# Performance work log

Measured on AMD Instinct MI355X. Metric: run time of the kernel, lower is better.

Reference implementation:

```python
import jax, jax.numpy as jnp
import numpy as np

N = 100000   # nodes
E = 3200000  # edges (avg degree 32)
F_IN = 128   # node feature dim (lazy in_channels)
C = 16       # GAT out_channels, heads=1
ED = 2       # edge_dim
B = 512      # graphs in batch
OUT_X = 64; OUT_Y = 64; ROT = 4
EPS = 1e-5


def _bn(x, g, b):
    # BatchNorm1d in training mode: biased batch variance, eps=1e-5
    mu = x.mean(0, keepdims=True)
    var = x.var(0, keepdims=True)
    return g * (x - mu) * jax.lax.rsqrt(var + EPS) + b


def _gat(x, src, dst, edge_attr, W, We, att_s, att_d, att_e, bias):
    # PyG GATConv, heads=1: self-loops added with fill_value='mean' edge attrs
    n = x.shape[0]
    deg = jax.ops.segment_sum(jnp.ones_like(dst, jnp.float32), dst, num_segments=n)
    loop_attr = jax.ops.segment_sum(edge_attr, dst, num_segments=n) / jnp.maximum(deg, 1.0)[:, None]
    idx = jnp.arange(n)
    src_f = jnp.concatenate([src, idx])
    dst_f = jnp.concatenate([dst, idx])
    ea = jnp.concatenate([edge_attr, loop_attr], axis=0)  # [E+N, ED]
    h = x @ W                      # [N, C]
    a_s = h @ att_s                # [N]
    a_d = h @ att_d                # [N]
    a_e = (ea @ We) @ att_e        # [E+N]
    logits = jax.nn.leaky_relu(a_s[src_f] + a_d[dst_f] + a_e, 0.2)
    m = jax.ops.segment_max(logits, dst_f, num_segments=n)  # every node has a self-loop
    ex = jnp.exp(logits - m[dst_f])
    alpha = ex / jax.ops.segment_sum(ex, dst_f, num_segments=n)[dst_f]
    return jax.ops.segment_sum(alpha[:, None] * h[src_f], dst_f, num_segments=n) + bias


def _glorot(k, shp):
    lim = float(np.sqrt(6.0 / (shp[0] + shp[1])))
    return jax.random.uniform(k, shp, jnp.float32, -lim, lim)


def setup_inputs() -> dict:
    key = jax.random.key(0)
    k = jax.random.split(key, 48)
    d = {}
    d['x'] = jax.random.normal(k[0], (N, F_IN), jnp.float32)
    d['edge_index'] = jax.random.randint(k[1], (2, E), 0, N)
    d['edge_attr'] = jax.random.normal(k[2], (E, ED), jnp.float32)
    d['batch'] = jnp.sort(jax.random.randint(k[3], (N,), 0, B))
    # gat1
    d['W1'] = _glorot(k[4], (F_IN, C)); d['We1'] = _glorot(k[5], (ED, C))
    d['as1'] = 0.1 * jax.random.normal(k[6], (C,)); d['ad1'] = 0.1 * jax.random.normal(k[7], (C,))
    d['ae1'] = 0.1 * jax.random.normal(k[8], (C,)); d['b1'] = jnp.zeros((C,), jnp.float32)
    # norm1 (BatchNorm on nodes)
    d['g1'] = 1.0 + 0.1 * jax.random.normal(k[9], (C,)); d['bb1'] = 0.1 * jax.random.normal(k[10], (C,))
    # gat2
    d['W2'] = _glorot(k[11], (C, C)); d['We2'] = _glorot(k[12], (ED, C))
    d['as2'] = 0.1 * jax.random.normal(k[13], (C,)); d['ad2'] = 0.1 * jax.random.normal(k[14], (C,))
    d['ae2'] = 0.1 * jax.random.normal(k[15], (C,)); d['b2'] = jnp.zeros((C,), jnp.float32)
    # D2RL MLP tail
    d['gL1'] = 1.0 + 0.1 * jax.random.normal(k[16], (C,)); d['bL1'] = 0.1 * jax.random.normal(k[17], (C,))
    d['Wl1'] = _glorot(k[18], (C, C)); d['bl1'] = 0.1 * jax.random.normal(k[19], (C,))
    d['gL2'] = 1.0 + 0.1 * jax.random.normal(k[20], (2 * C,)); d['bL2'] = 0.1 * jax.random.normal(k[21], (2 * C,))
    d['Wl2'] = _glorot(k[22], (2 * C, C)); d['bl2'] = 0.1 * jax.random.normal(k[23], (C,))
    d['gL3'] = 1.0 + 0.1 * jax.random.normal(k[24], (2 * C,)); d['bL3'] = 0.1 * jax.random.normal(k[25], (2 * C,))
    d['Wl3'] = _glorot(k[26], (2 * C, C)); d['bl3'] = 0.1 * jax.random.normal(k[27], (C,))
    d['Wx'] = _glorot(k[28], (C, OUT_X)); d['bx'] = 0.1 * jax.random.normal(k[29], (OUT_X,))
    d['Wy'] = _glorot(k[30], (C, OUT_Y)); d['by'] = 0.1 * jax.random.normal(k[31], (OUT_Y,))
    d['Wr'] = _glorot(k[32], (C, ROT)); d['br'] = 0.1 * jax.random.normal(k[33], (ROT,))
    return d


def reference(x, edge_index, edge_attr, batch,
              W1, We1, as1, ad1, ae1, b1, g1, bb1,
              W2, We2, as2, ad2, ae2, b2,
              gL1, bL1, Wl1, bl1, gL2, bL2, Wl2, bl2, gL3, bL3, Wl3, bl3,
              Wx, bx, Wy, by, Wr, br):
    src, dst = edge_index[0], edge_index[1]
    h = jax.nn.relu(_gat(x, src, dst, edge_attr, W1, We1, as1, ad1, ae1, b1))
    h = _bn(h, g1, bb1)
    h = jax.nn.relu(_gat(h, src, dst, edge_attr, W2, We2, as2, ad2, ae2, b2))
    # MeanAggregation over graphs
    cnt = jax.ops.segment_sum(jnp.ones((h.shape[0],), jnp.float32), batch, num_segments=B)
    xe = jax.ops.segment_sum(h, batch, num_segments=B) / jnp.maximum(cnt, 1.0)[:, None]  # [B, C]
    z = _bn(xe, gL1, bL1)
    z = jax.nn.relu(z @ Wl1 + bl1)
    z = _bn(jnp.concatenate([z, xe], axis=1), gL2, bL2)
    z = jax.nn.relu(z @ Wl2 + bl2)
    z = _bn(jnp.concatenate([z, xe], axis=1), gL3, bL3)
    z = jax.nn.relu(z @ Wl3 + bl3)
    xx = jax.nn.softmax(z @ Wx + bx, axis=1)
    y = jax.nn.softmax(z @ Wy + by, axis=1)
    rot = jax.nn.softmax(z @ Wr + br, axis=1)
    return (xx, y, rot)
```

## Files before the change

### kernel.cpp

```cpp
#include <hip/hip_runtime.h>
#include <hip/hip_fp16.h>
#include <math.h>

#define C 16
#define FIN 128

typedef unsigned int u32x2 __attribute__((ext_vector_type(2)));

__global__ __launch_bounds__(256) void k_gemm1(
    const float* __restrict__ x, const float* __restrict__ W,
    const float* __restrict__ asw, const float* __restrict__ adw,
    __half* __restrict__ hh, float* __restrict__ a_s, float* __restrict__ a_d, int n) {
  __shared__ float xs[64 * 129];
  __shared__ float Ws[FIN * C];
  __shared__ float pAs[4][64], pAd[4][64];
  int t = threadIdx.x;
  int node0 = blockIdx.x * 64;
  for (int i = t; i < FIN * C; i += 256) Ws[i] = W[i];
  for (int i = t; i < 64 * FIN; i += 256) {
    int r = i >> 7, c = i & 127;
    int node = node0 + r;
    xs[r * 129 + c] = (node < n) ? x[(size_t)node * FIN + c] : 0.f;
  }
  __syncthreads();
  int nn = t & 63, cg = (t >> 6) * 4, grp = t >> 6;
  float a0 = 0.f, a1 = 0.f, a2 = 0.f, a3 = 0.f;
  const float* xr = &xs[nn * 129];
  #pragma unroll 8
  for (int k = 0; k < FIN; ++k) {
    float xv = xr[k];
    const float* wr = &Ws[k * C + cg];
    a0 += xv * wr[0]; a1 += xv * wr[1]; a2 += xv * wr[2]; a3 += xv * wr[3];
  }
  int node = node0 + nn;
  if (node < n) {
    __half2 p0 = __floats2half2_rn(a0, a1), p1 = __floats2half2_rn(a2, a3);
    unsigned u0, u1;
    memcpy(&u0, &p0, 4); memcpy(&u1, &p1, 4);
    *(uint2*)(hh + (size_t)node * 16 + cg) = make_uint2(u0, u1);
  }
  pAs[grp][nn] = a0 * asw[cg] + a1 * asw[cg + 1] + a2 * asw[cg + 2] + a3 * asw[cg + 3];
  pAd[grp][nn] = a0 * adw[cg] + a1 * adw[cg + 1] + a2 * adw[cg + 2] + a3 * adw[cg + 3];
  __syncthreads();
  if (t < 64 && node0 + t < n) {
    a_s[node0 + t] = pAs[0][t] + pAs[1][t] + pAs[2][t] + pAs[3][t];
    a_d[node0 + t] = pAd[0][t] + pAd[1][t] + pAd[2][t] + pAd[3][t];
  }
}

__global__ __launch_bounds__(256) void k_hist_rank(
    const int* __restrict__ dst, int* __restrict__ counts,
    int* __restrict__ rank, int ne) {
  int e = blockIdx.x * 256 + threadIdx.x;
  if (e < ne) rank[e] = atomicAdd(&counts[dst[e]], 1);
}

__global__ __launch_bounds__(512) void k_scan1(const int* __restrict__ counts,
                                               int* __restrict__ bsum, int n) {
  __shared__ int sd[512];
  int i = blockIdx.x * 512 + threadIdx.x;
  sd[threadIdx.x] = (i < n) ? counts[i] : 0;
  __syncthreads();
  for (int s = 256; s > 0; s >>= 1) {
    if (threadIdx.x < s) sd[threadIdx.x] += sd[threadIdx.x + s];
    __syncthreads();
  }
  if (threadIdx.x == 0) bsum[blockIdx.x] = sd[0];
}

__global__ __launch_bounds__(512) void k_scan2(int* __restrict__ bsum,
                                               int* __restrict__ offs,
                                               int nblk, int n) {
  __shared__ int sd[512];
  int t = threadIdx.x;
  int v = (t < nblk) ? bsum[t] : 0;
  sd[t] = v;
  __syncthreads();
  for (int off = 1; off < 512; off <<= 1) {
    int x = (t >= off) ? sd[t - off] : 0;
    __syncthreads();
    sd[t] += x;
    __syncthreads();
  }
  if (t < nblk) bsum[t] = sd[t] - v;
  if (t == nblk - 1) offs[n] = sd[t];
}

__global__ __launch_bounds__(512) void k_scan3(const int* __restrict__ counts,
                                               const int* __restrict__ bsum,
                                               int* __restrict__ offs, int n) {
  __shared__ int sd[512];
  int t = threadIdx.x;
  int i = blockIdx.x * 512 + t;
  int v = (i < n) ? counts[i] : 0;
  sd[t] = v;
  __syncthreads();
  for (int off = 1; off < 512; off <<= 1) {
    int x = (t >= off) ? sd[t - off] : 0;
    __syncthreads();
    sd[t] += x;
    __syncthreads();
  }
  if (i < n) offs[i] = bsum[blockIdx.x] + sd[t] - v;
}

__global__ __launch_bounds__(256) void k_scatter(
    const int* __restrict__ src, const int* __restrict__ dst,
    const float2* __restrict__ ea, const int* __restrict__ offs,
    const int* __restrict__ rank,
    const float* __restrict__ We1, const float* __restrict__ ae1,
    const float* __restrict__ We2, const float* __restrict__ ae2,
    uint2* __restrict__ bucket, int ne) {
  int e = blockIdx.x * 256 + threadIdx.x;
  if (e >= ne) return;
  float w01 = 0.f, w11 = 0.f, w02 = 0.f, w12 = 0.f;
  #pragma unroll
  for (int c = 0; c < C; ++c) {
    w01 += We1[c] * ae1[c]; w11 += We1[C + c] * ae1[c];
    w02 += We2[c] * ae2[c]; w12 += We2[C + c] * ae2[c];
  }
  int d = dst[e];
  float2 a = ea[e];
  __half2 hp = __floats2half2_rn(a.x * w01 + a.y * w11, a.x * w02 + a.y * w12);
  unsigned hb;
  memcpy(&hb, &hp, 4);
  bucket[offs[d] + rank[e]] = make_uint2((unsigned)src[e], hb);
}

__global__ __launch_bounds__(256) void k_gather(
    const uint2* __restrict__ bucket, const int* __restrict__ offs,
    const float* __restrict__ a_s, const float* __restrict__ a_d,
    const __half* __restrict__ hh, const float* __restrict__ bias,
    float* __restrict__ outv, float* __restrict__ bnsum, float* __restrict__ bnsq,
    int lay, int do_bn, int n) {
  __shared__ float sbn[32];
  int t = threadIdx.x;
  if (t < 32) sbn[t] = 0.f;
  __syncthreads();

  int node = blockIdx.x * 16 + (t >> 4);
  int l = t & 15, f = l & 1, p = l >> 1;

  float acc[8];
  #pragma unroll
  for (int j = 0; j < 8; ++j) acc[j] = 0.f;
  float den = 0.f, ssum = 0.f;
  int o0 = 0, o1 = 0;
  float adi = 0.f, asi = 0.f;
  if (node < n) {
    o0 = offs[node]; o1 = offs[node + 1];
    adi = a_d[node]; asi = a_s[node];
    int e = o0 + p;
    u32x2 r = {0u, 0u};
    if (e < o1) r = __builtin_nontemporal_load((const u32x2*)(bucket + e));
    while (e < o1) {
      int en = e + 8;
      u32x2 rn = {0u, 0u};
      if (en < o1) rn = __builtin_nontemporal_load((const u32x2*)(bucket + en));
      int s = (int)r.x;
      unsigned scb = r.y;
      __half2 sc2;
      memcpy(&sc2, &scb, 4);
      float se = lay ? __high2float(sc2) : __low2float(sc2);
      float asv = a_s[s];
      uint4 hv = *(const uint4*)(hh + ((size_t)s << 4) + (f << 3));
      float lg = asv + adi + se;
      lg = lg > 0.f ? lg : 0.2f * lg;
      float ex = __expf(lg);
      den += ex; ssum += se;
      __half2 t0, t1, t2, t3;
      memcpy(&t0, &hv.x, 4); memcpy(&t1, &hv.y, 4);
      memcpy(&t2, &hv.z, 4); memcpy(&t3, &hv.w, 4);
      float2 g0 = __half22float2(t0), g1 = __half22float2(t1);
      float2 g2 = __half22float2(t2), g3 = __half22float2(t3);
      acc[0] += ex * g0.x; acc[1] += ex * g0.y;
      acc[2] += ex * g1.x; acc[3] += ex * g1.y;
      acc[4] += ex * g2.x; acc[5] += ex * g2.y;
      acc[6] += ex * g3.x; acc[7] += ex * g3.y;
      r = rn; e = en;
    }
  }
  #pragma unroll
  for (int off = 2; off <= 8; off <<= 1) {
    den += __shfl_xor(den, off);
    ssum += __shfl_xor(ssum, off);
    #pragma unroll
    for (int j = 0; j < 8; ++j) acc[j] += __shfl_xor(acc[j], off);
  }

  float v[8];
  #pragma unroll
  for (int j = 0; j < 8; ++j) v[j] = 0.f;
  if (node < n) {
    float dgc = fmaxf((float)(o1 - o0), 1.f);
    float lg = asi + adi + ssum / dgc;
    lg = lg > 0.f ? lg : 0.2f * lg;
    float exs = __expf(lg);
    uint4 hv = *(const uint4*)(hh + ((size_t)node << 4) + (f << 3));
    __half2 t0, t1, t2, t3;
    memcpy(&t0, &hv.x, 4); memcpy(&t1, &hv.y, 4);
    memcpy(&t2, &hv.z, 4); memcpy(&t3, &hv.w, 4);
    float2 g0 = __half22float2(t0), g1 = __half22float2(t1);
    float2 g2 = __half22float2(t2), g3 = __half22float2(t3);
    float hs[8] = {g0.x, g0.y, g1.x, g1.y, g2.x, g2.y, g3.x, g3.y};
    float inv = 1.f / (den + exs);
    const float* bp = bias + f * 8;
    #pragma unroll
    for (int j = 0; j < 8; ++j)
      v[j] = fmaxf((acc[j] + exs * hs[j]) * inv + bp[j], 0.f);
    if (p == 0) {
      float4* op = (float4*)(outv + ((size_t)node << 4));
      op[f * 2]     = make_float4(v[0], v[1], v[2], v[3]);
      op[f * 2 + 1] = make_float4(v[4], v[5], v[6], v[7]);
    }
  }

  if (do_bn) {
    float sv[8], qv[8];
    bool act = (node < n) && (p == 0);
    #pragma unroll
    for (int j = 0; j < 8; ++j) {
      sv[j] = act ? v[j] : 0.f;
      qv[j] = sv[j] * sv[j];
    }
    #pragma unroll
    for (int j = 0; j < 8; ++j) {
      sv[j] += __shfl_down(sv[j], 32); qv[j] += __shfl_down(qv[j], 32);
      sv[j] += __shfl_down(sv[j], 16); qv[j] += __shfl_down(qv[j], 16);
    }
    if ((t & 63) < 2) {
      #pragma unroll
      for (int j = 0; j < 8; ++j) {
        atomicAdd(&sbn[f * 8 + j], sv[j]);
        atomicAdd(&sbn[16 + f * 8 + j], qv[j]);
      }
    }
    __syncthreads();
    if (t < 16) atomicAdd(&bnsum[t], sbn[t]);
    else if (t < 32) atomicAdd(&bnsq[t - 16], sbn[t]);
  }
}

__global__ void k_bnp(const float* __restrict__ bnsum, const float* __restrict__ bnsq,
                      const float* __restrict__ g, const float* __restrict__ bb,
                      float* __restrict__ scale, float* __restrict__ shift, float invn) {
  int c = threadIdx.x;
  if (c >= C) return;
  float mean = bnsum[c] * invn;
  float var = bnsq[c] * invn - mean * mean;
  float s = g[c] * rsqrtf(var + 1e-5f);
  scale[c] = s; shift[c] = bb[c] - mean * s;
}

__global__ __launch_bounds__(256) void k_node2(
    const float* __restrict__ outv, const float* __restrict__ scale,
    const float* __restrict__ shift, const float* __restrict__ W2,
    const float* __restrict__ asw, const float* __restrict__ adw,
    __half* __restrict__ hh, float* __restrict__ a_s, float* __restrict__ a_d, int n) {
  __shared__ float w2s[C * C];
  if (threadIdx.x < C * C) w2s[threadIdx.x] = W2[threadIdx.x];
  __syncthreads();
  int i = blockIdx.x * 256 + threadIdx.x;
  if (i >= n) return;
  float hn[C];
  #pragma unroll
  for (int c = 0; c < C; ++c) hn[c] = outv[(size_t)i * C + c] * scale[c] + shift[c];
  float h2[C];
  #pragma unroll
  for (int j = 0; j < C; ++j) {
    float acc = 0.f;
    #pragma unroll
    for (int c = 0; c < C; ++c) acc += hn[c] * w2s[c * C + j];
    h2[j] = acc;
  }
  float hs = 0.f, hd = 0.f;
  #pragma unroll
  for (int j = 0; j < C; ++j) { hs += h2[j] * asw[j]; hd += h2[j] * adw[j]; }
  a_s[i] = hs; a_d[i] = hd;
  unsigned wbits[8];
  #pragma unroll
  for (int j = 0; j < 8; ++j) {
    __half2 hq = __floats2half2_rn(h2[2 * j], h2[2 * j + 1]);
    memcpy(&wbits[j], &hq, 4);
  }
  uint4* hp = (uint4*)(hh + (size_t)i * 16);
  hp[0] = make_uint4(wbits[0], wbits[1], wbits[2], wbits[3]);
  hp[1] = make_uint4(wbits[4], wbits[5], wbits[6], wbits[7]);
}

__global__ void k_gstart(const int* __restrict__ batch, int* __restrict__ gs,
                         int n, int B_) {
  int g = blockIdx.x * blockDim.x + threadIdx.x;
  if (g > B_) return;
  if (g == B_) { gs[B_] = n; return; }
  int lo = 0, hi = n;
  while (lo < hi) { int mid = (lo + hi) >> 1; if (batch[mid] < g) lo = mid + 1; else hi = mid; }
  gs[g] = lo;
}

__global__ __launch_bounds__(256) void k_xe(
    const float* __restrict__ outv, const int* __restrict__ gs,
    float* __restrict__ xe, int B_) {
  int wave = blockIdx.x * 4 + (threadIdx.x >> 6);
  if (wave >= B_) return;
  int lane = threadIdx.x & 63;
  int c = lane & 15, sub = lane >> 4;
  int base = gs[wave], end = gs[wave + 1];
  float s = 0.f;
  for (int n0 = base + sub; n0 < end; n0 += 4) s += outv[(size_t)n0 * C + c];
  s += __shfl_down(s, 32);
  s += __shfl_down(s, 16);
  if (lane < 16) xe[(size_t)wave * C + c] = s / fmaxf((float)(end - base), 1.f);
}

__global__ __launch_bounds__(512) void k_tail_z3(
    const float* __restrict__ xe_in,
    const float* __restrict__ gL1, const float* __restrict__ bL1,
    const float* __restrict__ Wl1, const float* __restrict__ bl1,
    const float* __restrict__ gL2, const float* __restrict__ bL2,
    const float* __restrict__ Wl2, const float* __restrict__ bl2,
    const float* __restrict__ gL3, const float* __restrict__ bL3,
    const float* __restrict__ Wl3, const float* __restrict__ bl3,
    float* __restrict__ z3buf, int B_) {
  __shared__ float ssum[2 * C], ssq[2 * C], sc[2 * C], sh[2 * C];
  int t = threadIdx.x;
  float invB = 1.f / (float)B_;
  float xe[C];
  #pragma unroll
  for (int c = 0; c < C; ++c) xe[c] = xe_in[(size_t)t * C + c];

  if (t < 2 * C) { ssum[t] = 0.f; ssq[t] = 0.f; }
  __syncthreads();
  #pragma unroll
  for (int c = 0; c < C; ++c) {
    float s = xe[c], q = xe[c] * xe[c];
    for (int o = 32; o > 0; o >>= 1) { s += __shfl_down(s, o); q += __shfl_down(q, o); }
    if ((t & 63) == 0) { atomicAdd(&ssum[c], s); atomicAdd(&ssq[c], q); }
  }
  __syncthreads();
  if (t < C) {
    float mean = ssum[t] * invB, var = ssq[t] * invB - mean * mean;
    float s = gL1[t] * rsqrtf(var + 1e-5f);
    sc[t] = s; sh[t] = bL1[t] - mean * s;
  }
  __syncthreads();
  float z[C];
  #pragma unroll
  for (int j = 0; j < C; ++j) {
    float acc = bl1[j];
    #pragma unroll
    for (int c = 0; c < C; ++c) acc += (xe[c] * sc[c] + sh[c]) * Wl1[c * C + j];
    z[j] = fmaxf(acc, 0.f);
  }
  __syncthreads();

  if (t < 2 * C) { ssum[t] = 0.f; ssq[t] = 0.f; }
  __syncthreads();
  #pragma unroll
  for (int c = 0; c < C; ++c) {
    float s = z[c], q = z[c] * z[c];
    for (int o = 32; o > 0; o >>= 1) { s += __shfl_down(s, o); q += __shfl_down(q, o); }
    if ((t & 63) == 0) { atomicAdd(&ssum[c], s); atomicAdd(&ssq[c], q); }
    float s2 = xe[c], q2 = xe[c] * xe[c];
    for (int o = 32; o > 0; o >>= 1) { s2 += __shfl_down(s2, o); q2 += __shfl_down(q2, o); }
    if ((t & 63) == 0) { atomicAdd(&ssum[C + c], s2); atomicAdd(&ssq[C + c], q2); }
  }
  __syncthreads();
  if (t < 2 * C) {
    float mean = ssum[t] * invB, var = ssq[t] * invB - mean * mean;
    float s = gL2[t] * rsqrtf(var + 1e-5f);
    sc[t] = s; sh[t] = bL2[t] - mean * s;
  }
  __syncthreads();
  float z2[C];
  #pragma unroll
  for (int j = 0; j < C; ++j) {
    float acc = bl2[j];
    #pragma unroll
    for (int c = 0; c < C; ++c) acc += (z[c] * sc[c] + sh[c]) * Wl2[c * C + j];
    #pragma unroll
    for (int c = 0; c < C; ++c) acc += (xe[c] * sc[C + c] + sh[C + c]) * Wl2[(C + c) * C + j];
    z2[j] = fmaxf(acc, 0.f);
  }
  __syncthreads();

  if (t < 2 * C) { ssum[t] = 0.f; ssq[t] = 0.f; }
  __syncthreads();
  #pragma unroll
  for (int c = 0; c < C; ++c) {
    float s = z2[c], q = z2[c] * z2[c];
    for (int o = 32; o > 0; o >>= 1) { s += __shfl_down(s, o); q += __shfl_down(q, o); }
    if ((t & 63) == 0) { atomicAdd(&ssum[c], s); atomicAdd(&ssq[c], q); }
    float s2 = xe[c], q2 = xe[c] * xe[c];
    for (int o = 32; o > 0; o >>= 1) { s2 += __shfl_down(s2, o); q2 += __shfl_down(q2, o); }
    if ((t & 63) == 0) { atomicAdd(&ssum[C + c], s2); atomicAdd(&ssq[C + c], q2); }
  }
  __syncthreads();
  if (t < 2 * C) {
    float mean = ssum[t] * invB, var = ssq[t] * invB - mean * mean;
    float s = gL3[t] * rsqrtf(var + 1e-5f);
    sc[t] = s; sh[t] = bL3[t] - mean * s;
  }
  __syncthreads();
  #pragma unroll
  for (int j = 0; j < C; ++j) {
    float acc = bl3[j];
    #pragma unroll
    for (int c = 0; c < C; ++c) acc += (z2[c] * sc[c] + sh[c]) * Wl3[c * C + j];
    #pragma unroll
    for (int c = 0; c < C; ++c) acc += (xe[c] * sc[C + c] + sh[C + c]) * Wl3[(C + c) * C + j];
    z3buf[(size_t)t * C + j] = fmaxf(acc, 0.f);
  }
}

__global__ __launch_bounds__(256) void k_heads(
    const float* __restrict__ z3buf,
    const float* __restrict__ Wx, const float* __restrict__ bx,
    const float* __restrict__ Wy, const float* __restrict__ by,
    const float* __restrict__ Wr, const float* __restrict__ br,
    float* __restrict__ out, int B_) {
  int wv = blockIdx.x * 4 + (threadIdx.x >> 6);
  if (wv >= B_) return;
  int lane = threadIdx.x & 63;
  float z[C];
  #pragma unroll
  for (int c = 0; c < C; ++c) z[c] = z3buf[(size_t)wv * C + c];

  float ax = bx[lane];
  #pragma unroll
  for (int c = 0; c < C; ++c) ax += z[c] * Wx[c * 64 + lane];
  float m = ax;
  #pragma unroll
  for (int o = 32; o > 0; o >>= 1) m = fmaxf(m, __shfl_xor(m, o));
  float e = __expf(ax - m);
  float s = e;
  #pragma unroll
  for (int o = 32; o > 0; o >>= 1) s += __shfl_xor(s, o);
  out[(size_t)wv * 64 + lane] = e / s;

  float ay = by[lane];
  #pragma unroll
  for (int c = 0; c < C; ++c) ay += z[c] * Wy[c * 64 + lane];
  m = ay;
  #pragma unroll
  for (int o = 32; o > 0; o >>= 1) m = fmaxf(m, __shfl_xor(m, o));
  e = __expf(ay - m);
  s = e;
  #pragma unroll
  for (int o = 32; o > 0; o >>= 1) s += __shfl_xor(s, o);
  out[(size_t)B_ * 64 + (size_t)wv * 64 + lane] = e / s;

  if (lane < 4) {
    float ar = br[lane];
    #pragma unroll
    for (int c = 0; c < C; ++c) ar += z[c] * Wr[c * 4 + lane];
    float mr = ar;
    mr = fmaxf(mr, __shfl_xor(mr, 1));
    mr = fmaxf(mr, __shfl_xor(mr, 2));
    float er = __expf(ar - mr);
    float sr = er;
    sr += __shfl_xor(sr, 1);
    sr += __shfl_xor(sr, 2);
    out[(size_t)B_ * 128 + (size_t)wv * 4 + lane] = er / sr;
  }
}

extern "C" void kernel_launch(void* const* d_in, const int* in_sizes, int n_in,
                              void* d_out, int out_size, void* d_ws, size_t ws_size,
                              hipStream_t stream) {
  const float* x     = (const float*)d_in[0];
  const int*   eidx  = (const int*)d_in[1];
  const float* eattr = (const float*)d_in[2];
  const int*   batch = (const int*)d_in[3];
  const float* W1  = (const float*)d_in[4];
  const float* We1 = (const float*)d_in[5];
  const float* as1 = (const float*)d_in[6];
  const float* ad1 = (const float*)d_in[7];
  const float* ae1 = (const float*)d_in[8];
  const float* b1  = (const float*)d_in[9];
  const float* g1  = (const float*)d_in[10];
  const float* bb1 = (const float*)d_in[11];
  const float* W2  = (const float*)d_in[12];
  const float* We2 = (const float*)d_in[13];
  const float* as2 = (const float*)d_in[14];
  const float* ad2 = (const float*)d_in[15];
  const float* ae2 = (const float*)d_in[16];
  const float* b2  = (const float*)d_in[17];
  const float* gL1 = (const float*)d_in[18];
  const float* bL1 = (const float*)d_in[19];
  const float* Wl1 = (const float*)d_in[20];
  const float* bl1 = (const float*)d_in[21];
  const float* gL2 = (const float*)d_in[22];
  const float* bL2 = (const float*)d_in[23];
  const float* Wl2 = (const float*)d_in[24];
  const float* bl2 = (const float*)d_in[25];
  const float* gL3 = (const float*)d_in[26];
  const float* bL3 = (const float*)d_in[27];
  const float* Wl3 = (const float*)d_in[28];
  const float* bl3 = (const float*)d_in[29];
  const float* Wx  = (const float*)d_in[30];
  const float* bx  = (const float*)d_in[31];
  const float* Wy  = (const float*)d_in[32];
  const float* by  = (const float*)d_in[33];
  const float* Wr  = (const float*)d_in[34];
  const float* br  = (const float*)d_in[35];

  int N = in_sizes[3];
  int E = in_sizes[2] / 2;
  int B = out_size / 132;
  int nblk = (N + 511) / 512;

  char* w = (char*)d_ws;
  size_t o = 0;
  auto alloc = [&](size_t bytes) { char* p = w + o; o += (bytes + 15) & ~15ull; return p; };
  uint2*  bucket = (uint2*)alloc((size_t)E * 8);
  int*    rank   = (int*)alloc((size_t)E * 4);
  __half* hh     = (__half*)alloc((size_t)N * C * 2);
  float*  outv   = (float*)alloc((size_t)N * C * 4);
  float*  a_s    = (float*)alloc((size_t)N * 4);
  float*  a_d    = (float*)alloc((size_t)N * 4);
  int*    counts = (int*)alloc((size_t)N * 4);
  int*    offs   = (int*)alloc((size_t)(N + 4) * 4);
  int*    bsum   = (int*)alloc((size_t)(nblk + 4) * 4);
  float*  bn     = (float*)alloc(64 * 4);
  float*  xe     = (float*)alloc((size_t)B * C * 4);
  int*    gs     = (int*)alloc((size_t)(B + 4) * 4);
  float*  z3buf  = (float*)alloc((size_t)B * C * 4);

  const int* src = eidx;
  const int* dst = eidx + E;
  int ebl = (E + 255) / 256;
  int nbl = (N + 255) / 256;

  hipMemsetAsync(counts, 0, (size_t)N * 4, stream);
  hipMemsetAsync(bn, 0, 32 * 4, stream);

  k_gemm1<<<(N + 63) / 64, 256, 0, stream>>>(x, W1, as1, ad1, hh, a_s, a_d, N);
  k_hist_rank<<<ebl, 256, 0, stream>>>(dst, counts, rank, E);
  k_scan1<<<nblk, 512, 0, stream>>>(counts, bsum, N);
  k_scan2<<<1, 512, 0, stream>>>(bsum, offs, nblk, N);
  k_scan3<<<nblk, 512, 0, stream>>>(counts, bsum, offs, N);
  k_scatter<<<ebl, 256, 0, stream>>>(src, dst, (const float2*)eattr, offs, rank,
                                     We1, ae1, We2, ae2, bucket, E);
  k_gather<<<(N + 15) / 16, 256, 0, stream>>>(bucket, offs, a_s, a_d, hh, b1,
                                              outv, bn, bn + 16, 0, 1, N);
  k_bnp<<<1, 64, 0, stream>>>(bn, bn + 16, g1, bb1, bn + 32, bn + 48, 1.f / (float)N);
  k_node2<<<nbl, 256, 0, stream>>>(outv, bn + 32, bn + 48, W2, as2, ad2, hh, a_s, a_d, N);
  k_gather<<<(N + 15) / 16, 256, 0, stream>>>(bucket, offs, a_s, a_d, hh, b2,
                                              outv, bn, bn + 16, 1, 0, N);
  k_gstart<<<(B + 1 + 255) / 256, 256, 0, stream>>>(batch, gs, N, B);
  k_xe<<<(B + 3) / 4, 256, 0, stream>>>(outv, gs, xe, B);
  k_tail_z3<<<1, B, 0, stream>>>(xe, gL1, bL1, Wl1, bl1, gL2, bL2, Wl2, bl2,
                                 gL3, bL3, Wl3, bl3, z3buf, B);
  k_heads<<<(B + 3) / 4, 256, 0, stream>>>(z3buf, Wx, bx, Wy, by, Wr, br,
                                           (float*)d_out, B);
}
```

Before: 777.5 us.

## Assign one wavefront per node in GAT gather instead of sixteen lanes

The gather kernel now maps a full 64-lane wavefront to each destination node, so 32 edges are processed per iteration instead of 8. Out-of-range lanes are masked with clamped loads, the manual software prefetch is dropped, the shuffle reduction is widened to 32 lanes, and the BN partial sums switch to direct shared atomics. The aim is more memory-level parallelism per node and fewer loop trips. With an average degree of 32 most lanes stay busy, but low-degree nodes waste lanes and there are four times as many blocks.

```diff
diff --git a/kernel.cpp b/kernel.cpp
--- a/kernel.cpp
+++ b/kernel.cpp
@@ -138,8 +138,8 @@
   if (t < 32) sbn[t] = 0.f;
   __syncthreads();
 
-  int node = blockIdx.x * 16 + (t >> 4);
-  int l = t & 15, f = l & 1, p = l >> 1;
+  int node = blockIdx.x * 4 + (t >> 6);
+  int l = t & 63, p = l >> 1, f = l & 1;
 
   float acc[8];
   #pragma unroll
@@ -150,13 +150,11 @@
   if (node < n) {
     o0 = offs[node]; o1 = offs[node + 1];
     adi = a_d[node]; asi = a_s[node];
-    int e = o0 + p;
-    u32x2 r = {0u, 0u};
-    if (e < o1) r = __builtin_nontemporal_load((const u32x2*)(bucket + e));
-    while (e < o1) {
-      int en = e + 8;
-      u32x2 rn = {0u, 0u};
-      if (en < o1) rn = __builtin_nontemporal_load((const u32x2*)(bucket + en));
+    for (int base = o0; base < o1; base += 32) {
+      int e = base + p;
+      bool val = e < o1;
+      int ee = val ? e : (o1 - 1);
+      u32x2 r = __builtin_nontemporal_load((const u32x2*)(bucket + ee));
       int s = (int)r.x;
       unsigned scb = r.y;
       __half2 sc2;
@@ -166,8 +164,9 @@
       uint4 hv = *(const uint4*)(hh + ((size_t)s << 4) + (f << 3));
       float lg = asv + adi + se;
       lg = lg > 0.f ? lg : 0.2f * lg;
-      float ex = __expf(lg);
-      den += ex; ssum += se;
+      float ex = val ? __expf(lg) : 0.f;
+      den += ex;
+      ssum += val ? se : 0.f;
       __half2 t0, t1, t2, t3;
       memcpy(&t0, &hv.x, 4); memcpy(&t1, &hv.y, 4);
       memcpy(&t2, &hv.z, 4); memcpy(&t3, &hv.w, 4);
@@ -177,11 +176,10 @@
       acc[2] += ex * g1.x; acc[3] += ex * g1.y;
       acc[4] += ex * g2.x; acc[5] += ex * g2.y;
       acc[6] += ex * g3.x; acc[7] += ex * g3.y;
-      r = rn; e = en;
     }
   }
   #pragma unroll
-  for (int off = 2; off <= 8; off <<= 1) {
+  for (int off = 2; off <= 32; off <<= 1) {
     den += __shfl_xor(den, off);
     ssum += __shfl_xor(ssum, off);
     #pragma unroll
@@ -216,23 +214,12 @@
   }
 
   if (do_bn) {
-    float sv[8], qv[8];
     bool act = (node < n) && (p == 0);
-    #pragma unroll
-    for (int j = 0; j < 8; ++j) {
-      sv[j] = act ? v[j] : 0.f;
-      qv[j] = sv[j] * sv[j];
-    }
-    #pragma unroll
-    for (int j = 0; j < 8; ++j) {
-      sv[j] += __shfl_down(sv[j], 32); qv[j] += __shfl_down(qv[j], 32);
-      sv[j] += __shfl_down(sv[j], 16); qv[j] += __shfl_down(qv[j], 16);
-    }
-    if ((t & 63) < 2) {
+    if (act) {
       #pragma unroll
       for (int j = 0; j < 8; ++j) {
-        atomicAdd(&sbn[f * 8 + j], sv[j]);
-        atomicAdd(&sbn[16 + f * 8 + j], qv[j]);
+        atomicAdd(&sbn[f * 8 + j], v[j]);
+        atomicAdd(&sbn[16 + f * 8 + j], v[j] * v[j]);
       }
     }
     __syncthreads();
@@ -542,12 +529,12 @@
   k_scan3<<<nblk, 512, 0, stream>>>(counts, bsum, offs, N);
   k_scatter<<<ebl, 256, 0, stream>>>(src, dst, (const float2*)eattr, offs, rank,
                                      We1, ae1, We2, ae2, bucket, E);
-  k_gather<<<(N + 15) / 16, 256, 0, stream>>>(bucket, offs, a_s, a_d, hh, b1,
-                                              outv, bn, bn + 16, 0, 1, N);
+  k_gather<<<(N + 3) / 4, 256, 0, stream>>>(bucket, offs, a_s, a_d, hh, b1,
+                                            outv, bn, bn + 16, 0, 1, N);
   k_bnp<<<1, 64, 0, stream>>>(bn, bn + 16, g1, bb1, bn + 32, bn + 48, 1.f / (float)N);
   k_node2<<<nbl, 256, 0, stream>>>(outv, bn + 32, bn + 48, W2, as2, ad2, hh, a_s, a_d, N);
-  k_gather<<<(N + 15) / 16, 256, 0, stream>>>(bucket, offs, a_s, a_d, hh, b2,
-                                              outv, bn, bn + 16, 1, 0, N);
+  k_gather<<<(N + 3) / 4, 256, 0, stream>>>(bucket, offs, a_s, a_d, hh, b2,
+                                            outv, bn, bn + 16, 1, 0, N);
   k_gstart<<<(B + 1 + 255) / 256, 256, 0, stream>>>(batch, gs, N, B);
   k_xe<<<(B + 3) / 4, 256, 0, stream>>>(outv, gs, xe, B);
   k_tail_z3<<<1, B, 0, stream>>>(xe, gL1, bL1, Wl1, bl1, gL2, bL2, Wl2, bl2,
```

New measurement: 1.326 ms. 70.6% more time.
